# Optimization experiments

Hardware: AMD Instinct MI355X
Metric: run time of the kernel (lower is better)

Reference implementation:

```python
import jax, jax.numpy as jnp
import numpy as np

B, D, L, E, R = 16384, 512, 3, 4, 128

def setup_inputs() -> dict:
    key = jax.random.key(0)
    ks = jax.random.split(key, 6)
    scale = 0.05  # keep tanh in its non-saturated regime, like glorot-ish init
    return {
        "x":  jax.random.normal(ks[0], (B, D), dtype=jnp.float32),
        "Us": jax.random.normal(ks[1], (L, E, D, R), dtype=jnp.float32) * scale,
        "Cs": jax.random.normal(ks[2], (L, E, R, R), dtype=jnp.float32) * scale,
        "Vs": jax.random.normal(ks[3], (L, E, D, R), dtype=jnp.float32) * scale,
        "G":  jax.random.normal(ks[4], (L, E, D), dtype=jnp.float32) * scale,
        "b":  jnp.zeros((L, D), dtype=jnp.float32),
    }

def reference(x, Us, Cs, Vs, G, b):
    # x: (B, D). Original keeps x as (B, D, 1); we drop the trailing singleton.
    x0 = x
    xl = x
    num_layers = Us.shape[0]
    for i in range(num_layers):  # small fixed layer count
        U, C, V, g, bias = Us[i], Cs[i], Vs[i], G[i], b[i]
        # per-expert low-rank bilinear transform, fused over experts via einsum
        xv = jnp.tanh(jnp.einsum('edr,bd->ber', V, xl))       # (B, E, R)
        xc = jnp.tanh(jnp.einsum('ers,bes->ber', C, xv))      # (B, E, R)
        xu = jnp.einsum('edr,ber->bed', U, xc)                # (B, E, D)
        cross = x0[:, None, :] * (xu + bias[None, None, :])   # (B, E, D) experts
        # gating: Dense(1, no bias) per expert -> scores (B, E, 1)
        scores = jnp.einsum('bd,ed->be', xl, g)[..., None]
        # NOTE: original applies softmax over the LAST axis of (B, E, 1),
        # a singleton axis, so gates are all ones. Reproduced faithfully.
        gate = jax.nn.softmax(scores, axis=-1)                # (B, E, 1) of ones
        moe = jnp.einsum('bed,be->bd', cross, gate[..., 0])   # (B, D)
        xl = moe + xl
    return xl
```

## Files before the change

kernel.cpp:

```cpp
#include <hip/hip_runtime.h>
#include <hip/hip_bf16.h>

#define BATCH  16384
#define DIM    512
#define NLAYER 3
#define NEXP   4
#define RANK   128

typedef __bf16 bf16_t;
typedef bf16_t bf16x8 __attribute__((ext_vector_type(8)));
typedef bf16_t bf16x4 __attribute__((ext_vector_type(4)));
typedef float  f32x4  __attribute__((ext_vector_type(4)));

__device__ __forceinline__ float tanh_fast(float x) {
    float e = __expf(2.0f * x);
    return 1.0f - 2.0f * __builtin_amdgcn_rcpf(e + 1.0f);
}
__device__ __forceinline__ int swz(int row, int b) { return b ^ ((row & 7) << 4); }

__device__ __forceinline__ bf16x8 ldsr(const bf16_t* base, int row, int kb) {
    return *(const bf16x8*)((const char*)base + row * 1024 + swz(row, kb));
}
__device__ __forceinline__ void ldsw2(bf16_t* base, int row, int cb, bf16_t v) {
    *(bf16_t*)((char*)base + row * 1024 + swz(row, cb)) = v;
}
__device__ __forceinline__ void barrier_lds() {
    asm volatile("s_waitcnt lgkmcnt(0)" ::: "memory");
    __builtin_amdgcn_s_barrier();
}

__global__ void prep_pack(const float* __restrict__ Vs,
                          const float* __restrict__ Us,
                          const float* __restrict__ Cs,
                          bf16_t* __restrict__ Vp,
                          bf16_t* __restrict__ Up,
                          bf16_t* __restrict__ Cp) {
    int t = blockIdx.x * 256 + threadIdx.x;
    if (t < 98304) {
        int lane = t & 63, ni = (t >> 6) & 1, ks = (t >> 7) & 15,
            wn = (t >> 11) & 15, l = t >> 15;
        int c = wn * 32 + ni * 16 + (lane & 15), e = c >> 7, r = c & 127;
        int d0 = ks * 32 + (lane >> 4) * 8;
        const float* src = Vs + ((size_t)(l * NEXP + e) * DIM + d0) * RANK + r;
        bf16x8 v;
        #pragma unroll
        for (int j = 0; j < 8; ++j) v[j] = (bf16_t)src[j * RANK];
        *(bf16x8*)(Vp + (size_t)t * 8) = v;
    } else if (t < 196608) {
        int q = t - 98304;
        int lane = q & 63, ni = (q >> 6) & 1, ks = (q >> 7) & 15,
            wn = (q >> 11) & 15, l = q >> 15;
        int d = wn * 32 + ni * 16 + (lane & 15);
        int k0 = ks * 32 + (lane >> 4) * 8, e = k0 >> 7, r0 = k0 & 127;
        const float* src = Us + ((size_t)(l * NEXP + e) * DIM + d) * RANK + r0;
        bf16x8 v;
        #pragma unroll
        for (int j = 0; j < 8; ++j) v[j] = (bf16_t)src[j];
        *(bf16x8*)(Up + (size_t)q * 8) = v;
    } else if (t < 221184) {
        int q = t - 196608;
        int lane = q & 63, ni = (q >> 6) & 1, k4 = (q >> 7) & 3,
            wn = (q >> 9) & 15, l = q >> 13;
        int c = wn * 32 + ni * 16 + (lane & 15);
        int e = wn >> 2, rp = c & 127;
        int s0 = k4 * 32 + (lane >> 4) * 8;
        const float* src = Cs + ((size_t)(l * NEXP + e) * RANK + rp) * RANK + s0;
        bf16x8 v;
        #pragma unroll
        for (int j = 0; j < 8; ++j) v[j] = (bf16_t)src[j];
        *(bf16x8*)(Cp + (size_t)q * 8) = v;
    }
}


__global__ __launch_bounds__(1024, 4)
void fused3(const float* __restrict__ x,
            const bf16_t* __restrict__ Vp,
            const bf16_t* __restrict__ Up,
            const bf16_t* __restrict__ Cp,
            const float* __restrict__ bb,
            float* __restrict__ out)
{
    __shared__ __align__(16) char smem[131072];
    bf16_t* bufA = (bf16_t*)smem;
    bf16_t* bufB = (bf16_t*)(smem + 65536);

    const int tid  = threadIdx.x;
    const int lane = tid & 63;
    const int wn   = tid >> 6;
    const int lr   = lane & 15;
    const int lg   = lane >> 4;
    const int m0   = blockIdx.x * 64;

    #pragma unroll
    for (int it = 0; it < 8; ++it) {
        int q = tid + 1024 * it;
        int row = q >> 7, c4 = (q & 127) << 2;
        float4 v = *(const float4*)(x + (size_t)(m0 + row) * DIM + c4);
        bf16x4 b4 = { (bf16_t)v.x, (bf16_t)v.y, (bf16_t)v.z, (bf16_t)v.w };
        *(bf16x4*)((char*)bufA + row * 1024 + swz(row, c4 * 2)) = b4;
    }
    f32x4  xlf[4][2];
    bf16x4 x0r[4][2];
    #pragma unroll
    for (int mi = 0; mi < 4; ++mi)
        #pragma unroll
        for (int ni = 0; ni < 2; ++ni)
            #pragma unroll
            for (int j = 0; j < 4; ++j) {
                int row = mi * 16 + lg * 4 + j, col = wn * 32 + ni * 16 + lr;
                float v = x[(size_t)(m0 + row) * DIM + col];
                xlf[mi][ni][j] = v;
                x0r[mi][ni][j] = (bf16_t)v;
            }
    barrier_lds();

    #pragma unroll 1
    for (int l = 0; l < NLAYER; ++l) {
        bf16_t* xl_b = (l & 1) ? bufB : bufA;
        bf16_t* xv_b = (l & 1) ? bufA : bufB;

        const bf16_t* Vw = Vp + (((size_t)l * 16 + wn) << 14) + lane * 8;
        const bf16_t* Uw = Up + (((size_t)l * 16 + wn) << 14) + lane * 8;
        const bf16_t* Cw = Cp + (((size_t)l * 16 + wn) << 12) + lane * 8;

        {
            f32x4 a1[4][2] = {};
            const bf16_t* vp = Vw;
            #pragma unroll 2
            for (int ks = 0; ks < 16; ++ks) {
                bf16x8 bv[2];
                bv[0] = *(const bf16x8*)(vp);
                bv[1] = *(const bf16x8*)(vp + 512);
                vp += 1024;
                #pragma unroll
                for (int mi = 0; mi < 4; ++mi) {
                    bf16x8 av = ldsr(xl_b, mi * 16 + lr, ks * 64 + lg * 16);
                    #pragma unroll
                    for (int ni = 0; ni < 2; ++ni)
                        a1[mi][ni] = __builtin_amdgcn_mfma_f32_16x16x32_bf16(
                            av, bv[ni], a1[mi][ni], 0, 0, 0);
                }
            }
            #pragma unroll
            for (int mi = 0; mi < 4; ++mi)
                #pragma unroll
                for (int ni = 0; ni < 2; ++ni)
                    #pragma unroll
                    for (int j = 0; j < 4; ++j)
                        ldsw2(xv_b, mi * 16 + lg * 4 + j,
                              (wn * 32 + ni * 16 + lr) * 2,
                              (bf16_t)tanh_fast(a1[mi][ni][j]));
            barrier_lds();
        }

        {
            const int eb = (wn >> 2) * 256;
            f32x4 a2[4][2] = {};
            #pragma unroll 2
            for (int k4 = 0; k4 < 4; ++k4) {
                bf16x8 bv[2];
                bv[0] = *(const bf16x8*)(Cw + (k4 * 2 + 0) * 512);
                bv[1] = *(const bf16x8*)(Cw + (k4 * 2 + 1) * 512);
                #pragma unroll
                for (int mi = 0; mi < 4; ++mi) {
                    bf16x8 av = ldsr(xv_b, mi * 16 + lr, eb + k4 * 64 + lg * 16);
                    #pragma unroll
                    for (int ni = 0; ni < 2; ++ni)
                        a2[mi][ni] = __builtin_amdgcn_mfma_f32_16x16x32_bf16(
                            av, bv[ni], a2[mi][ni], 0, 0, 0);
                }
            }
            #pragma unroll
            for (int mi = 0; mi < 4; ++mi)
                #pragma unroll
                for (int ni = 0; ni < 2; ++ni)
                    #pragma unroll
                    for (int j = 0; j < 4; ++j)
                        ldsw2(xl_b, mi * 16 + lg * 4 + j,
                              (wn * 32 + ni * 16 + lr) * 2,
                              (bf16_t)tanh_fast(a2[mi][ni][j]));
            barrier_lds();
        }

        {
            f32x4 a3[4][2] = {};
            const bf16_t* up = Uw;
            #pragma unroll 2
            for (int ks = 0; ks < 16; ++ks) {
                bf16x8 bv[2];
                bv[0] = *(const bf16x8*)(up);
                bv[1] = *(const bf16x8*)(up + 512);
                up += 1024;
                #pragma unroll
                for (int mi = 0; mi < 4; ++mi) {
                    bf16x8 av = ldsr(xl_b, mi * 16 + lr, ks * 64 + lg * 16);
                    #pragma unroll
                    for (int ni = 0; ni < 2; ++ni)
                        a3[mi][ni] = __builtin_amdgcn_mfma_f32_16x16x32_bf16(
                            av, bv[ni], a3[mi][ni], 0, 0, 0);
                }
            }

            const float* bl = bb + l * DIM;
            #pragma unroll
            for (int ni = 0; ni < 2; ++ni) {
                int col = wn * 32 + ni * 16 + lr;
                float b4v = 4.0f * bl[col];
                #pragma unroll
                for (int mi = 0; mi < 4; ++mi)
                    #pragma unroll
                    for (int j = 0; j < 4; ++j)
                        xlf[mi][ni][j] +=
                            (float)x0r[mi][ni][j] * (a3[mi][ni][j] + b4v);
            }
        }

        if (l < NLAYER - 1) {
            #pragma unroll
            for (int mi = 0; mi < 4; ++mi)
                #pragma unroll
                for (int ni = 0; ni < 2; ++ni)
                    #pragma unroll
                    for (int j = 0; j < 4; ++j)
                        ldsw2(xv_b, mi * 16 + lg * 4 + j,
                              (wn * 32 + ni * 16 + lr) * 2,
                              (bf16_t)xlf[mi][ni][j]);
            barrier_lds();
        }
    }

    #pragma unroll
    for (int mi = 0; mi < 4; ++mi)
        #pragma unroll
        for (int ni = 0; ni < 2; ++ni)
            #pragma unroll
            for (int j = 0; j < 4; ++j) {
                int row = mi * 16 + lg * 4 + j, col = wn * 32 + ni * 16 + lr;
                out[(size_t)(m0 + row) * DIM + col] = xlf[mi][ni][j];
            }
}


extern "C" void kernel_launch(void* const* d_in, const int* in_sizes, int n_in,
                              void* d_out, int out_size, void* d_ws, size_t ws_size,
                              hipStream_t stream) {
    const float* x  = (const float*)d_in[0];
    const float* Us = (const float*)d_in[1];
    const float* Cs = (const float*)d_in[2];
    const float* Vs = (const float*)d_in[3];
    const float* bb = (const float*)d_in[5];
    float* out = (float*)d_out;

    bf16_t* Vp = (bf16_t*)d_ws;
    bf16_t* Up = Vp + 786432;
    bf16_t* Cp = Up + 786432;

    prep_pack<<<864, 256, 0, stream>>>(Vs, Us, Cs, Vp, Up, Cp);
    fused3<<<BATCH / 64, 1024, 0, stream>>>(x, Vp, Up, Cp, bb, out);
}
```

Baseline: 129.6 us.

## Split fused three-layer kernel into one launch per layer

Replaces the single kernel that ran all three layers with xl held in registers by a per-layer kernel launched three times. Each launch re-reads xl and x0 from global memory in fp32 and writes xl back. This drops the register-resident xlf/x0r state and the per-layer LDS rewrite, which may lower register pressure and keep x0 in fp32 rather than bf16. The cost is extra global traffic, two more launches, and a layer-to-layer dependency carried through global memory.

```diff
diff --git a/kernel.cpp b/kernel.cpp
--- a/kernel.cpp
+++ b/kernel.cpp
@@ -73,13 +73,14 @@
 }
 
 
-__global__ __launch_bounds__(1024, 4)
-void fused3(const float* __restrict__ x,
-            const bf16_t* __restrict__ Vp,
-            const bf16_t* __restrict__ Up,
-            const bf16_t* __restrict__ Cp,
-            const float* __restrict__ bb,
-            float* __restrict__ out)
+__global__ __launch_bounds__(1024)
+void k_layer(const float* xl_in,
+             const float* __restrict__ x0,
+             const bf16_t* __restrict__ Vw0,
+             const bf16_t* __restrict__ Uw0,
+             const bf16_t* __restrict__ Cw0,
+             const float* __restrict__ bl,
+             float* xl_out)
 {
     __shared__ __align__(16) char smem[131072];
     bf16_t* bufA = (bf16_t*)smem;
@@ -96,149 +97,104 @@
     for (int it = 0; it < 8; ++it) {
         int q = tid + 1024 * it;
         int row = q >> 7, c4 = (q & 127) << 2;
-        float4 v = *(const float4*)(x + (size_t)(m0 + row) * DIM + c4);
+        float4 v = *(const float4*)(xl_in + (size_t)(m0 + row) * DIM + c4);
         bf16x4 b4 = { (bf16_t)v.x, (bf16_t)v.y, (bf16_t)v.z, (bf16_t)v.w };
         *(bf16x4*)((char*)bufA + row * 1024 + swz(row, c4 * 2)) = b4;
     }
-    f32x4  xlf[4][2];
-    bf16x4 x0r[4][2];
-    #pragma unroll
-    for (int mi = 0; mi < 4; ++mi)
-        #pragma unroll
-        for (int ni = 0; ni < 2; ++ni)
-            #pragma unroll
-            for (int j = 0; j < 4; ++j) {
-                int row = mi * 16 + lg * 4 + j, col = wn * 32 + ni * 16 + lr;
-                float v = x[(size_t)(m0 + row) * DIM + col];
-                xlf[mi][ni][j] = v;
-                x0r[mi][ni][j] = (bf16_t)v;
+    barrier_lds();
+
+    const bf16_t* Vw = Vw0 + ((size_t)wn << 14) + lane * 8;
+    const bf16_t* Uw = Uw0 + ((size_t)wn << 14) + lane * 8;
+    const bf16_t* Cw = Cw0 + ((size_t)wn << 12) + lane * 8;
+
+    {
+        f32x4 a1[4][2] = {};
+        const bf16_t* vp = Vw;
+        #pragma unroll 2
+        for (int ks = 0; ks < 16; ++ks) {
+            bf16x8 bv0 = *(const bf16x8*)(vp);
+            bf16x8 bv1 = *(const bf16x8*)(vp + 512);
+            vp += 1024;
+            #pragma unroll
+            for (int mi = 0; mi < 4; ++mi) {
+                bf16x8 av = ldsr(bufA, mi * 16 + lr, ks * 64 + lg * 16);
+                a1[mi][0] = __builtin_amdgcn_mfma_f32_16x16x32_bf16(
+                    av, bv0, a1[mi][0], 0, 0, 0);
+                a1[mi][1] = __builtin_amdgcn_mfma_f32_16x16x32_bf16(
+                    av, bv1, a1[mi][1], 0, 0, 0);
             }
-    barrier_lds();
-
-    #pragma unroll 1
-    for (int l = 0; l < NLAYER; ++l) {
-        bf16_t* xl_b = (l & 1) ? bufB : bufA;
-        bf16_t* xv_b = (l & 1) ? bufA : bufB;
-
-        const bf16_t* Vw = Vp + (((size_t)l * 16 + wn) << 14) + lane * 8;
-        const bf16_t* Uw = Up + (((size_t)l * 16 + wn) << 14) + lane * 8;
-        const bf16_t* Cw = Cp + (((size_t)l * 16 + wn) << 12) + lane * 8;
-
-        {
-            f32x4 a1[4][2] = {};
-            const bf16_t* vp = Vw;
-            #pragma unroll 2
-            for (int ks = 0; ks < 16; ++ks) {
-                bf16x8 bv[2];
-                bv[0] = *(const bf16x8*)(vp);
-                bv[1] = *(const bf16x8*)(vp + 512);
-                vp += 1024;
+        }
+        #pragma unroll
+        for (int mi = 0; mi < 4; ++mi)
+            #pragma unroll
+            for (int ni = 0; ni < 2; ++ni)
                 #pragma unroll
-                for (int mi = 0; mi < 4; ++mi) {
-                    bf16x8 av = ldsr(xl_b, mi * 16 + lr, ks * 64 + lg * 16);
-                    #pragma unroll
-                    for (int ni = 0; ni < 2; ++ni)
-                        a1[mi][ni] = __builtin_amdgcn_mfma_f32_16x16x32_bf16(
-                            av, bv[ni], a1[mi][ni], 0, 0, 0);
-                }
+                for (int j = 0; j < 4; ++j)
+                    ldsw2(bufB, mi * 16 + lg * 4 + j,
+                          (wn * 32 + ni * 16 + lr) * 2,
+                          (bf16_t)tanh_fast(a1[mi][ni][j]));
+        barrier_lds();
+    }
+
+    {
+        const int eb = (wn >> 2) * 256;
+        f32x4 a2[4][2] = {};
+        #pragma unroll 2
+        for (int k4 = 0; k4 < 4; ++k4) {
+            bf16x8 bv0 = *(const bf16x8*)(Cw + (k4 * 2 + 0) * 512);
+            bf16x8 bv1 = *(const bf16x8*)(Cw + (k4 * 2 + 1) * 512);
+            #pragma unroll
+            for (int mi = 0; mi < 4; ++mi) {
+                bf16x8 av = ldsr(bufB, mi * 16 + lr, eb + k4 * 64 + lg * 16);
+                a2[mi][0] = __builtin_amdgcn_mfma_f32_16x16x32_bf16(
+                    av, bv0, a2[mi][0], 0, 0, 0);
+                a2[mi][1] = __builtin_amdgcn_mfma_f32_16x16x32_bf16(
+                    av, bv1, a2[mi][1], 0, 0, 0);
             }
+        }
+        #pragma unroll
+        for (int mi = 0; mi < 4; ++mi)
+            #pragma unroll
+            for (int ni = 0; ni < 2; ++ni)
+                #pragma unroll
+                for (int j = 0; j < 4; ++j)
+                    ldsw2(bufA, mi * 16 + lg * 4 + j,
+                          (wn * 32 + ni * 16 + lr) * 2,
+                          (bf16_t)tanh_fast(a2[mi][ni][j]));
+        barrier_lds();
+    }
+
+    {
+        f32x4 a3[4][2] = {};
+        const bf16_t* up = Uw;
+        #pragma unroll 2
+        for (int ks = 0; ks < 16; ++ks) {
+            bf16x8 bv0 = *(const bf16x8*)(up);
+            bf16x8 bv1 = *(const bf16x8*)(up + 512);
+            up += 1024;
+            #pragma unroll
+            for (int mi = 0; mi < 4; ++mi) {
+                bf16x8 av = ldsr(bufA, mi * 16 + lr, ks * 64 + lg * 16);
+                a3[mi][0] = __builtin_amdgcn_mfma_f32_16x16x32_bf16(
+                    av, bv0, a3[mi][0], 0, 0, 0);
+                a3[mi][1] = __builtin_amdgcn_mfma_f32_16x16x32_bf16(
+                    av, bv1, a3[mi][1], 0, 0, 0);
+            }
+        }
+
+        #pragma unroll
+        for (int ni = 0; ni < 2; ++ni) {
+            int col = wn * 32 + ni * 16 + lr;
+            float b4v = 4.0f * bl[col];
             #pragma unroll
             for (int mi = 0; mi < 4; ++mi)
                 #pragma unroll
-                for (int ni = 0; ni < 2; ++ni)
-                    #pragma unroll
-                    for (int j = 0; j < 4; ++j)
-                        ldsw2(xv_b, mi * 16 + lg * 4 + j,
-                              (wn * 32 + ni * 16 + lr) * 2,
-                              (bf16_t)tanh_fast(a1[mi][ni][j]));
-            barrier_lds();
-        }
-
-        {
-            const int eb = (wn >> 2) * 256;
-            f32x4 a2[4][2] = {};
-            #pragma unroll 2
-            for (int k4 = 0; k4 < 4; ++k4) {
-                bf16x8 bv[2];
-                bv[0] = *(const bf16x8*)(Cw + (k4 * 2 + 0) * 512);
-                bv[1] = *(const bf16x8*)(Cw + (k4 * 2 + 1) * 512);
-                #pragma unroll
-                for (int mi = 0; mi < 4; ++mi) {
-                    bf16x8 av = ldsr(xv_b, mi * 16 + lr, eb + k4 * 64 + lg * 16);
-                    #pragma unroll
-                    for (int ni = 0; ni < 2; ++ni)
-                        a2[mi][ni] = __builtin_amdgcn_mfma_f32_16x16x32_bf16(
-                            av, bv[ni], a2[mi][ni], 0, 0, 0);
+                for (int j = 0; j < 4; ++j) {
+                    size_t idx = (size_t)(m0 + mi * 16 + lg * 4 + j) * DIM + col;
+                    xl_out[idx] = xl_in[idx] + x0[idx] * (a3[mi][ni][j] + b4v);
                 }
-            }
-            #pragma unroll
-            for (int mi = 0; mi < 4; ++mi)
-                #pragma unroll
-                for (int ni = 0; ni < 2; ++ni)
-                    #pragma unroll
-                    for (int j = 0; j < 4; ++j)
-                        ldsw2(xl_b, mi * 16 + lg * 4 + j,
-                              (wn * 32 + ni * 16 + lr) * 2,
-                              (bf16_t)tanh_fast(a2[mi][ni][j]));
-            barrier_lds();
-        }
-
-        {
-            f32x4 a3[4][2] = {};
-            const bf16_t* up = Uw;
-            #pragma unroll 2
-            for (int ks = 0; ks < 16; ++ks) {
-                bf16x8 bv[2];
-                bv[0] = *(const bf16x8*)(up);
-                bv[1] = *(const bf16x8*)(up + 512);
-                up += 1024;
-                #pragma unroll
-                for (int mi = 0; mi < 4; ++mi) {
-                    bf16x8 av = ldsr(xl_b, mi * 16 + lr, ks * 64 + lg * 16);
-                    #pragma unroll
-                    for (int ni = 0; ni < 2; ++ni)
-                        a3[mi][ni] = __builtin_amdgcn_mfma_f32_16x16x32_bf16(
-                            av, bv[ni], a3[mi][ni], 0, 0, 0);
-                }
-            }
-
-            const float* bl = bb + l * DIM;
-            #pragma unroll
-            for (int ni = 0; ni < 2; ++ni) {
-                int col = wn * 32 + ni * 16 + lr;
-                float b4v = 4.0f * bl[col];
-                #pragma unroll
-                for (int mi = 0; mi < 4; ++mi)
-                    #pragma unroll
-                    for (int j = 0; j < 4; ++j)
-                        xlf[mi][ni][j] +=
-                            (float)x0r[mi][ni][j] * (a3[mi][ni][j] + b4v);
-            }
-        }
-
-        if (l < NLAYER - 1) {
-            #pragma unroll
-            for (int mi = 0; mi < 4; ++mi)
-                #pragma unroll
-                for (int ni = 0; ni < 2; ++ni)
-                    #pragma unroll
-                    for (int j = 0; j < 4; ++j)
-                        ldsw2(xv_b, mi * 16 + lg * 4 + j,
-                              (wn * 32 + ni * 16 + lr) * 2,
-                              (bf16_t)xlf[mi][ni][j]);
-            barrier_lds();
-        }
-    }
-
-    #pragma unroll
-    for (int mi = 0; mi < 4; ++mi)
-        #pragma unroll
-        for (int ni = 0; ni < 2; ++ni)
-            #pragma unroll
-            for (int j = 0; j < 4; ++j) {
-                int row = mi * 16 + lg * 4 + j, col = wn * 32 + ni * 16 + lr;
-                out[(size_t)(m0 + row) * DIM + col] = xlf[mi][ni][j];
-            }
+        }
+    }
 }
 
 
@@ -257,5 +213,15 @@
     bf16_t* Cp = Up + 786432;
 
     prep_pack<<<864, 256, 0, stream>>>(Vs, Us, Cs, Vp, Up, Cp);
-    fused3<<<BATCH / 64, 1024, 0, stream>>>(x, Vp, Up, Cp, bb, out);
-}
+
+    for (int l = 0; l < NLAYER; ++l) {
+        k_layer<<<BATCH / 64, 1024, 0, stream>>>(
+            (l == 0) ? x : out,
+            x,
+            Vp + (size_t)l * 262144,
+            Up + (size_t)l * 262144,
+            Cp + (size_t)l * 65536,
+            bb + (size_t)l * DIM,
+            out);
+    }
+}
```

New measurement: 132.5 us. +2.2%, slower.
